# Kernel tuning notes

Measured on AMD Instinct MI355X. Metric: run time of the kernel, lower is better.

The kernel has to match this reference:

```python
import jax, jax.numpy as jnp
import numpy as np


def setup_inputs() -> dict:
    key = jax.random.key(0)
    kA, kB = jax.random.split(key)
    B, H, W, C = 1, 80, 80, 256  # NHWC backbone features; B must be 1 for the TF broadcast in the divide to be valid
    feature_A = jax.random.normal(kA, (B, H, W, C), dtype=jnp.float32)
    feature_B = jax.random.normal(kB, (B, H, W, C), dtype=jnp.float32)
    return {"feature_A": feature_A, "feature_B": feature_B}


def reference(feature_A, feature_B):
    # corr[b,i,j,k,l] = mean_c A[b,i,j,c] * B[b,k,l,c]
    # Expressed as a batched matmul instead of materializing the (H,W,H,W,C) intermediate.
    C = feature_A.shape[-1]
    corr = jnp.einsum('bijc,bklc->bijkl', feature_A, feature_B) / C  # [B,H,W,H,W]
    # penalty[b,i,j] = sqrt(sum_{k,l} corr^2)
    penalty = jnp.sqrt(jnp.sum(corr * corr, axis=(-1, -2)))  # [B,H,W]
    # Faithful to tf.math.divide: trailing-dim broadcasting of [B,H,W] against [B,H,W,H,W]
    # (valid because B == 1; penalty aligns to the (j,k,l) trailing axes exactly as in TF).
    return corr / penalty
```

## Files before the change

### kernel.cpp

```cpp
#include <hip/hip_runtime.h>

typedef __attribute__((ext_vector_type(8))) short bf16x8;
typedef __attribute__((ext_vector_type(4))) float f32x4;

#define M_TOT 6400
#define C_TOT 256
#define BM 128
#define BN 128
#define BK 32
#define GK_CHUNKS 20
#define GK_STEPS  10

#define VMCNT0 asm volatile("s_waitcnt vmcnt(0)" ::: "memory")
#define SBAR   __builtin_amdgcn_s_barrier()

__device__ __forceinline__ short f2bf(float f) {
    unsigned u = __float_as_uint(f);
    u = (u + 0x7fffu + ((u >> 16) & 1u)) >> 16;
    return (short)u;
}
__device__ __forceinline__ float bf2f(short s) {
    return __uint_as_float(((unsigned)(unsigned short)s) << 16);
}

__device__ __forceinline__ void gload16(const short* g, short* l) {
    __builtin_amdgcn_global_load_lds(
        (const __attribute__((address_space(1))) void*)g,
        (__attribute__((address_space(3))) void*)l, 16, 0, 0);
}


__global__ __launch_bounds__(256) void convert_bf16(const float* __restrict__ A,
                                                    const float* __restrict__ Bm,
                                                    short* __restrict__ Ab,
                                                    short* __restrict__ Bb)
{
    const int n8 = M_TOT * C_TOT / 8;
    for (int i = blockIdx.x * blockDim.x + threadIdx.x; i < 2 * n8;
         i += gridDim.x * blockDim.x) {
        const float* s = (i < n8) ? (A + (size_t)i * 8) : (Bm + (size_t)(i - n8) * 8);
        short* d       = (i < n8) ? (Ab + (size_t)i * 8) : (Bb + (size_t)(i - n8) * 8);
        const float4 v0 = reinterpret_cast<const float4*>(s)[0];
        const float4 v1 = reinterpret_cast<const float4*>(s)[1];
        bf16x8 w;
        w[0]=f2bf(v0.x); w[1]=f2bf(v0.y); w[2]=f2bf(v0.z); w[3]=f2bf(v0.w);
        w[4]=f2bf(v1.x); w[5]=f2bf(v1.y); w[6]=f2bf(v1.z); w[7]=f2bf(v1.w);
        *reinterpret_cast<bf16x8*>(d) = w;
    }
}

__global__ __launch_bounds__(256) void transpose_b(const float* __restrict__ Bm,
                                                   short* __restrict__ Bt)
{
    __shared__ __align__(16) short Lb[64][72];
    const int t  = threadIdx.x;
    const int n0 = blockIdx.x * 64;
    const int c0 = blockIdx.y * 64;
    const int r  = t >> 2;
    const int cb = (t & 3) * 16;

    const float4* src = reinterpret_cast<const float4*>(
        Bm + (size_t)(n0 + r) * C_TOT + c0 + cb);
    const float4 v0 = src[0], v1 = src[1], v2 = src[2], v3 = src[3];
    bf16x8 w0, w1;
    w0[0]=f2bf(v0.x); w0[1]=f2bf(v0.y); w0[2]=f2bf(v0.z); w0[3]=f2bf(v0.w);
    w0[4]=f2bf(v1.x); w0[5]=f2bf(v1.y); w0[6]=f2bf(v1.z); w0[7]=f2bf(v1.w);
    w1[0]=f2bf(v2.x); w1[1]=f2bf(v2.y); w1[2]=f2bf(v2.z); w1[3]=f2bf(v2.w);
    w1[4]=f2bf(v3.x); w1[5]=f2bf(v3.y); w1[6]=f2bf(v3.z); w1[7]=f2bf(v3.w);
    *reinterpret_cast<bf16x8*>(&Lb[r][cb])     = w0;
    *reinterpret_cast<bf16x8*>(&Lb[r][cb + 8]) = w1;
    __syncthreads();

    #pragma unroll
    for (int p = 0; p < 2; ++p) {
        const int q = t + p * 256;
        const int c = q >> 3;
        const int h = q & 7;
        bf16x8 w;
        #pragma unroll
        for (int j = 0; j < 8; ++j) w[j] = Lb[h * 8 + j][c];
        *reinterpret_cast<bf16x8*>(&Bt[(size_t)(c0 + c) * M_TOT + n0 + h * 8]) = w;
    }
}


__device__ __forceinline__ void stage_tiles_g(const short* __restrict__ A,
                                              const short* __restrict__ B,
                                              int m0, int n0, int k0,
                                              int lda, int ldb,
                                              short* As, short* Bs,
                                              int wave, int lane)
{
    #pragma unroll
    for (int t = 0; t < 2; ++t) {
        const int c  = (wave * 2 + t) * 64 + lane;
        const int r  = c >> 2;
        const int g  = c & 3;
        const int sg = g ^ ((r >> 1) & 3);
        gload16(A + (size_t)(m0 + r) * lda + k0 + sg * 8, As + (wave * 2 + t) * 512);
        gload16(B + (size_t)(n0 + r) * ldb + k0 + sg * 8, Bs + (wave * 2 + t) * 512);
    }
}

template<int KSTEPS>
__device__ __forceinline__ void gemm_tile_g(const short* __restrict__ A,
                                            const short* __restrict__ B,
                                            int m0, int n0, int kbase,
                                            int lda, int ldb, int tid,
                                            short (*Sm)[2][4096],
                                            f32x4 acc[4][4])
{
    const int lane = tid & 63;
    const int wave = tid >> 6;
    const int rl   = lane & 15;
    const int g_rd = lane >> 4;
    const int wr   = wave >> 1;
    const int wc   = wave & 1;

    stage_tiles_g(A, B, m0, n0, kbase, lda, ldb, &Sm[0][0][0], &Sm[0][1][0], wave, lane);
    VMCNT0; SBAR;

    #pragma unroll
    for (int kt = 0; kt < KSTEPS; ++kt) {
        const int cur = kt & 1;
        if (kt < KSTEPS - 1)
            stage_tiles_g(A, B, m0, n0, kbase + (kt + 1) * BK, lda, ldb,
                          &Sm[cur ^ 1][0][0], &Sm[cur ^ 1][1][0], wave, lane);

        bf16x8 af[4], bfr[4];
        #pragma unroll
        for (int mi = 0; mi < 4; ++mi) {
            const int r  = wr * 64 + mi * 16 + rl;
            const int sg = g_rd ^ ((r >> 1) & 3);
            af[mi] = *reinterpret_cast<const bf16x8*>(&Sm[cur][0][r * BK + sg * 8]);
        }
        #pragma unroll
        for (int ni = 0; ni < 4; ++ni) {
            const int r  = wc * 64 + ni * 16 + rl;
            const int sg = g_rd ^ ((r >> 1) & 3);
            bfr[ni] = *reinterpret_cast<const bf16x8*>(&Sm[cur][1][r * BK + sg * 8]);
        }
        #pragma unroll
        for (int mi = 0; mi < 4; ++mi)
            #pragma unroll
            for (int ni = 0; ni < 4; ++ni)
                acc[mi][ni] = __builtin_amdgcn_mfma_f32_16x16x32_bf16(
                    af[mi], bfr[ni], acc[mi][ni], 0, 0, 0);

        if (kt < KSTEPS - 1) { VMCNT0; SBAR; }
    }
}


__global__ __launch_bounds__(256) void gemm_G(const short* __restrict__ Bt,
                                              float* __restrict__ Gp)
{
    __shared__ __align__(16) short Sm[2][2][4096];
    const int tid = threadIdx.x;
    const int m0 = blockIdx.y * BM, n0 = blockIdx.x * BN;
    const int z  = blockIdx.z;
    f32x4 acc[4][4] = {};
    gemm_tile_g<GK_STEPS>(Bt, Bt, m0, n0, z * (M_TOT / GK_CHUNKS),
                          M_TOT, M_TOT, tid, Sm, acc);

    float* dst = Gp + (size_t)z * (C_TOT * C_TOT);
    const int lane = tid & 63, rl = lane & 15;
    const int wave = tid >> 6, wr = wave >> 1, wc = wave & 1;
    #pragma unroll
    for (int mi = 0; mi < 4; ++mi)
        #pragma unroll
        for (int i = 0; i < 4; ++i) {
            const int m = m0 + wr * 64 + mi * 16 + (lane >> 4) * 4 + i;
            #pragma unroll
            for (int ni = 0; ni < 4; ++ni)
                dst[m * C_TOT + n0 + wc * 64 + ni * 16 + rl] = acc[mi][ni][i];
        }
}

__global__ __launch_bounds__(256) void g_reduce(const float* __restrict__ Gp,
                                                short* __restrict__ Gb)
{
    const int i4 = blockIdx.x * 256 + threadIdx.x;
    float4 s = make_float4(0.f, 0.f, 0.f, 0.f);
    for (int z = 0; z < GK_CHUNKS; ++z) {
        const float4 v = reinterpret_cast<const float4*>(
            Gp + (size_t)z * (C_TOT * C_TOT))[i4];
        s.x += v.x; s.y += v.y; s.z += v.z; s.w += v.w;
    }
    short4 o;
    o.x = f2bf(s.x); o.y = f2bf(s.y); o.z = f2bf(s.z); o.w = f2bf(s.w);
    reinterpret_cast<short4*>(Gb)[i4] = o;
}

__global__ __launch_bounds__(256) void penalty_G(const short* __restrict__ Ab,
                                                 const short* __restrict__ Gb,
                                                 float* __restrict__ P)
{
    __shared__ __align__(16) short Sm[2][2][4096];
    __shared__ float q_lds[BM];
    const int tid = threadIdx.x;
    const int m0 = blockIdx.x * BM;
    const int lane = tid & 63, rl = lane & 15;
    const int wave = tid >> 6, wr = wave >> 1, wc = wave & 1;

    if (tid < BM) q_lds[tid] = 0.0f;
    __syncthreads();

    #pragma unroll
    for (int nt = 0; nt < 2; ++nt) {
        f32x4 acc[4][4] = {};
        gemm_tile_g<8>(Ab, Gb, m0, nt * BN, 0, C_TOT, C_TOT, tid, Sm, acc);
        const int n0 = nt * BN;
        #pragma unroll
        for (int mi = 0; mi < 4; ++mi)
            #pragma unroll
            for (int i = 0; i < 4; ++i) {
                const int m = m0 + wr * 64 + mi * 16 + (lane >> 4) * 4 + i;
                float s = 0.0f;
                #pragma unroll
                for (int ni = 0; ni < 4; ++ni) {
                    const int cp = n0 + wc * 64 + ni * 16 + rl;
                    s += acc[mi][ni][i] * bf2f(Ab[(size_t)m * C_TOT + cp]);
                }
                s += __shfl_xor(s, 1);
                s += __shfl_xor(s, 2);
                s += __shfl_xor(s, 4);
                s += __shfl_xor(s, 8);
                if (rl == 0) atomicAdd(&q_lds[m - m0], s);
            }
    }
    __syncthreads();
    if (tid < BM) P[m0 + tid] = q_lds[tid];
}


__global__ __launch_bounds__(256) void gemm_out(const short* __restrict__ Ab,
                                                const short* __restrict__ Bb,
                                                const float* __restrict__ P,
                                                float* __restrict__ out)
{
    __shared__ __align__(16) short Sm[2][2][4096];
    const int tid = threadIdx.x;
    const int lane = tid & 63, rl = lane & 15;
    const int wave = tid >> 6, wr = wave >> 1, wc = wave & 1;
    const int m0 = blockIdx.y * BM, n0 = blockIdx.x * BN;

    float rs[4];
    #pragma unroll
    for (int ni = 0; ni < 4; ++ni)
        rs[ni] = rsqrtf(P[n0 + wc * 64 + ni * 16 + rl]);

    f32x4 acc[4][4] = {};
    gemm_tile_g<8>(Ab, Bb, m0, n0, 0, C_TOT, C_TOT, tid, Sm, acc);

    SBAR;

    float* Es = reinterpret_cast<float*>(Sm) + wave * 1088;
    #pragma unroll
    for (int mi = 0; mi < 4; ++mi) {
        #pragma unroll
        for (int ni = 0; ni < 4; ++ni)
            #pragma unroll
            for (int i = 0; i < 4; ++i)
                Es[((lane >> 4) * 4 + i) * 68 + ni * 16 + rl] = acc[mi][ni][i] * rs[ni];
        #pragma unroll
        for (int it = 0; it < 4; ++it) {
            const int f   = it * 64 + lane;
            const int row = f >> 4;
            const int c4  = f & 15;
            const float4 v = *reinterpret_cast<const float4*>(&Es[row * 68 + c4 * 4]);
            const int m = m0 + wr * 64 + mi * 16 + row;
            *reinterpret_cast<float4*>(&out[(size_t)m * M_TOT + n0 + wc * 64 + c4 * 4]) = v;
        }
    }
}


__global__ __launch_bounds__(256) void gemm_penalty(const short* __restrict__ Ab,
                                                    const short* __restrict__ Bb,
                                                    float* __restrict__ P)
{
    __shared__ __align__(16) short Sm[2][2][4096];
    const int tid = threadIdx.x;
    const int m0 = blockIdx.y * BM, n0 = blockIdx.x * BN;
    f32x4 acc[4][4] = {};
    gemm_tile_g<8>(Ab, Bb, m0, n0, 0, C_TOT, C_TOT, tid, Sm, acc);

    const int lane = tid & 63, rl = lane & 15;
    const int wave = tid >> 6, wr = wave >> 1;
    #pragma unroll
    for (int mi = 0; mi < 4; ++mi) {
        #pragma unroll
        for (int i = 0; i < 4; ++i) {
            const int m = m0 + wr * 64 + mi * 16 + (lane >> 4) * 4 + i;
            float s = 0.0f;
            #pragma unroll
            for (int ni = 0; ni < 4; ++ni) {
                const float v = acc[mi][ni][i];
                s += v * v;
            }
            s += __shfl_xor(s, 1);
            s += __shfl_xor(s, 2);
            s += __shfl_xor(s, 4);
            s += __shfl_xor(s, 8);
            if (rl == 0) atomicAdd(&P[m], s);
        }
    }
}


__global__ __launch_bounds__(256) void corr_gemm(const float* __restrict__ A,
                                                 const float* __restrict__ Bm,
                                                 float* __restrict__ out,
                                                 float* __restrict__ penalty)
{
    __shared__ short As[BM * BK];
    __shared__ short Bs[BN * BK];

    const int tid  = threadIdx.x;
    const int lane = tid & 63;
    const int wave = tid >> 6;
    const int wr   = wave >> 1;
    const int wc   = wave & 1;
    const int m0   = blockIdx.y * BM;
    const int n0   = blockIdx.x * BN;
    const int g_rd = lane >> 4;
    const int rl   = lane & 15;

    f32x4 acc[4][4] = {};

    for (int k0 = 0; k0 < C_TOT; k0 += BK) {
        #pragma unroll
        for (int half = 0; half < 2; ++half) {
            const int cc = tid + half * 256;
            const int r  = cc >> 2;
            const int g  = cc & 3;
            const int sg = g ^ ((r >> 1) & 3);

            const float4* pa = reinterpret_cast<const float4*>(
                A + (size_t)(m0 + r) * C_TOT + k0 + g * 8);
            float4 a0 = pa[0], a1 = pa[1];
            bf16x8 wa;
            wa[0]=f2bf(a0.x); wa[1]=f2bf(a0.y); wa[2]=f2bf(a0.z); wa[3]=f2bf(a0.w);
            wa[4]=f2bf(a1.x); wa[5]=f2bf(a1.y); wa[6]=f2bf(a1.z); wa[7]=f2bf(a1.w);
            *reinterpret_cast<bf16x8*>(&As[r * BK + sg * 8]) = wa;

            const float4* pb = reinterpret_cast<const float4*>(
                Bm + (size_t)(n0 + r) * C_TOT + k0 + g * 8);
            float4 b0 = pb[0], b1 = pb[1];
            bf16x8 wb;
            wb[0]=f2bf(b0.x); wb[1]=f2bf(b0.y); wb[2]=f2bf(b0.z); wb[3]=f2bf(b0.w);
            wb[4]=f2bf(b1.x); wb[5]=f2bf(b1.y); wb[6]=f2bf(b1.z); wb[7]=f2bf(b1.w);
            *reinterpret_cast<bf16x8*>(&Bs[r * BK + sg * 8]) = wb;
        }
        __syncthreads();

        bf16x8 af[4], bfr[4];
        #pragma unroll
        for (int mi = 0; mi < 4; ++mi) {
            const int r  = wr * 64 + mi * 16 + rl;
            const int sg = g_rd ^ ((r >> 1) & 3);
            af[mi] = *reinterpret_cast<const bf16x8*>(&As[r * BK + sg * 8]);
        }
        #pragma unroll
        for (int ni = 0; ni < 4; ++ni) {
            const int r  = wc * 64 + ni * 16 + rl;
            const int sg = g_rd ^ ((r >> 1) & 3);
            bfr[ni] = *reinterpret_cast<const bf16x8*>(&Bs[r * BK + sg * 8]);
        }
        #pragma unroll
        for (int mi = 0; mi < 4; ++mi)
            #pragma unroll
            for (int ni = 0; ni < 4; ++ni)
                acc[mi][ni] = __builtin_amdgcn_mfma_f32_16x16x32_bf16(
                    af[mi], bfr[ni], acc[mi][ni], 0, 0, 0);
        __syncthreads();
    }

    const float inv_c = 1.0f / (float)C_TOT;
    #pragma unroll
    for (int mi = 0; mi < 4; ++mi) {
        #pragma unroll
        for (int i = 0; i < 4; ++i) {
            const int m = m0 + wr * 64 + mi * 16 + (lane >> 4) * 4 + i;
            float s = 0.0f;
            #pragma unroll
            for (int ni = 0; ni < 4; ++ni) {
                const float v = acc[mi][ni][i] * inv_c;
                out[(size_t)m * M_TOT + n0 + wc * 64 + ni * 16 + rl] = v;
                s += v * v;
            }
            s += __shfl_xor(s, 1);
            s += __shfl_xor(s, 2);
            s += __shfl_xor(s, 4);
            s += __shfl_xor(s, 8);
            if (rl == 0) atomicAdd(&penalty[m], s);
        }
    }
}

__global__ __launch_bounds__(256) void scale_k(float* __restrict__ out,
                                               const float* __restrict__ penalty)
{
    const unsigned cols4 = M_TOT / 4;
    const unsigned total = (unsigned)M_TOT * cols4;
    float4* o4 = reinterpret_cast<float4*>(out);
    const float4* p4 = reinterpret_cast<const float4*>(penalty);
    for (unsigned idx = blockIdx.x * blockDim.x + threadIdx.x; idx < total;
         idx += gridDim.x * blockDim.x) {
        const unsigned n4 = idx % cols4;
        const float4 p = p4[n4];
        float4 v = o4[idx];
        v.x *= rsqrtf(p.x);
        v.y *= rsqrtf(p.y);
        v.z *= rsqrtf(p.z);
        v.w *= rsqrtf(p.w);
        o4[idx] = v;
    }
}


extern "C" void kernel_launch(void* const* d_in, const int* in_sizes, int n_in,
                              void* d_out, int out_size, void* d_ws, size_t ws_size,
                              hipStream_t stream) {
    const float* A = (const float*)d_in[0];
    const float* B = (const float*)d_in[1];
    float* out     = (float*)d_out;

    const size_t mat_sh = (size_t)M_TOT * C_TOT;
    const size_t sz_ab  = mat_sh * sizeof(short);
    const size_t sz_gb  = (size_t)C_TOT * C_TOT * sizeof(short);
    const size_t sz_p   = (size_t)M_TOT * sizeof(float);
    const size_t sz_gp  = (size_t)GK_CHUNKS * C_TOT * C_TOT * sizeof(float);
    const size_t need_full = 3 * sz_ab + sz_gb + sz_p + sz_gp;
    const size_t need_mid  = 2 * sz_ab + sz_p;

    dim3 grid(M_TOT / BN, M_TOT / BM);

    if (ws_size >= need_full) {
        short* Ab = (short*)d_ws;
        short* Bb = Ab + mat_sh;
        short* Bt = Bb + mat_sh;
        short* Gb = Bt + mat_sh;
        float* P  = (float*)((char*)d_ws + 3 * sz_ab + sz_gb);
        float* Gp = (float*)((char*)d_ws + 3 * sz_ab + sz_gb + sz_p);

        convert_bf16<<<1600, 256, 0, stream>>>(A, B, Ab, Bb);
        transpose_b<<<dim3(M_TOT / 64, C_TOT / 64), 256, 0, stream>>>(B, Bt);
        gemm_G<<<dim3(2, 2, GK_CHUNKS), 256, 0, stream>>>(Bt, Gp);
        g_reduce<<<64, 256, 0, stream>>>(Gp, Gb);
        penalty_G<<<M_TOT / BM, 256, 0, stream>>>(Ab, Gb, P);
        gemm_out<<<grid, dim3(256), 0, stream>>>(Ab, Bb, P, out);
    } else if (ws_size >= need_mid) {
        short* Ab = (short*)d_ws;
        short* Bb = Ab + mat_sh;
        float* P  = (float*)(Bb + mat_sh);

        hipMemsetAsync(P, 0, sz_p, stream);
        convert_bf16<<<1600, 256, 0, stream>>>(A, B, Ab, Bb);
        gemm_penalty<<<grid, dim3(256), 0, stream>>>(Ab, Bb, P);
        gemm_out<<<grid, dim3(256), 0, stream>>>(Ab, Bb, P, out);
    } else {
        float* penalty = (float*)d_ws;
        hipMemsetAsync(penalty, 0, sz_p, stream);
        corr_gemm<<<grid, dim3(256), 0, stream>>>(A, B, out, penalty);
        scale_k<<<2048, 256, 0, stream>>>(out, penalty);
    }
}
```

Before: 89.86 us.

## Triple-buffer GEMM K-loop, remap gemm_out blocks across XCDs, fuse B conversion into transpose

```diff
diff --git a/kernel.cpp b/kernel.cpp
--- a/kernel.cpp
+++ b/kernel.cpp
@@ -8,10 +8,12 @@
 #define BM 128
 #define BN 128
 #define BK 32
+#define NTILE 50
 #define GK_CHUNKS 20
 #define GK_STEPS  10
 
 #define VMCNT0 asm volatile("s_waitcnt vmcnt(0)" ::: "memory")
+#define VMCNT4 asm volatile("s_waitcnt vmcnt(4)" ::: "memory")
 #define SBAR   __builtin_amdgcn_s_barrier()
 
 __device__ __forceinline__ short f2bf(float f) {
@@ -30,10 +32,25 @@
 }
 
 
-__global__ __launch_bounds__(256) void convert_bf16(const float* __restrict__ A,
-                                                    const float* __restrict__ Bm,
-                                                    short* __restrict__ Ab,
-                                                    short* __restrict__ Bb)
+__global__ __launch_bounds__(256) void convert_a(const float* __restrict__ A,
+                                                 short* __restrict__ Ab)
+{
+    const int n8 = M_TOT * C_TOT / 8;
+    for (int i = blockIdx.x * blockDim.x + threadIdx.x; i < n8;
+         i += gridDim.x * blockDim.x) {
+        const float4 v0 = reinterpret_cast<const float4*>(A + (size_t)i * 8)[0];
+        const float4 v1 = reinterpret_cast<const float4*>(A + (size_t)i * 8)[1];
+        bf16x8 w;
+        w[0]=f2bf(v0.x); w[1]=f2bf(v0.y); w[2]=f2bf(v0.z); w[3]=f2bf(v0.w);
+        w[4]=f2bf(v1.x); w[5]=f2bf(v1.y); w[6]=f2bf(v1.z); w[7]=f2bf(v1.w);
+        *reinterpret_cast<bf16x8*>(Ab + (size_t)i * 8) = w;
+    }
+}
+
+__global__ __launch_bounds__(256) void convert_ab(const float* __restrict__ A,
+                                                  const float* __restrict__ Bm,
+                                                  short* __restrict__ Ab,
+                                                  short* __restrict__ Bb)
 {
     const int n8 = M_TOT * C_TOT / 8;
     for (int i = blockIdx.x * blockDim.x + threadIdx.x; i < 2 * n8;
@@ -49,8 +66,9 @@
     }
 }
 
-__global__ __launch_bounds__(256) void transpose_b(const float* __restrict__ Bm,
-                                                   short* __restrict__ Bt)
+__global__ __launch_bounds__(256) void trans_b(const float* __restrict__ Bm,
+                                               short* __restrict__ Bb,
+                                               short* __restrict__ Bt)
 {
     __shared__ __align__(16) short Lb[64][72];
     const int t  = threadIdx.x;
@@ -69,6 +87,9 @@
     w1[4]=f2bf(v3.x); w1[5]=f2bf(v3.y); w1[6]=f2bf(v3.z); w1[7]=f2bf(v3.w);
     *reinterpret_cast<bf16x8*>(&Lb[r][cb])     = w0;
     *reinterpret_cast<bf16x8*>(&Lb[r][cb + 8]) = w1;
+    short* brow = Bb + (size_t)(n0 + r) * C_TOT + c0 + cb;
+    *reinterpret_cast<bf16x8*>(brow)     = w0;
+    *reinterpret_cast<bf16x8*>(brow + 8) = w1;
     __syncthreads();
 
     #pragma unroll
@@ -118,14 +139,18 @@
     const int wc   = wave & 1;
 
     stage_tiles_g(A, B, m0, n0, kbase, lda, ldb, &Sm[0][0][0], &Sm[0][1][0], wave, lane);
-    VMCNT0; SBAR;
+    if (KSTEPS > 1)
+        stage_tiles_g(A, B, m0, n0, kbase + BK, lda, ldb,
+                      &Sm[1][0][0], &Sm[1][1][0], wave, lane);
+    if (KSTEPS > 1) { VMCNT4; } else { VMCNT0; }
+    SBAR;
 
     #pragma unroll
     for (int kt = 0; kt < KSTEPS; ++kt) {
-        const int cur = kt & 1;
-        if (kt < KSTEPS - 1)
-            stage_tiles_g(A, B, m0, n0, kbase + (kt + 1) * BK, lda, ldb,
-                          &Sm[cur ^ 1][0][0], &Sm[cur ^ 1][1][0], wave, lane);
+        const int cur = kt % 3;
+        if (kt + 2 < KSTEPS)
+            stage_tiles_g(A, B, m0, n0, kbase + (kt + 2) * BK, lda, ldb,
+                          &Sm[(kt + 2) % 3][0][0], &Sm[(kt + 2) % 3][1][0], wave, lane);
 
         bf16x8 af[4], bfr[4];
         #pragma unroll
@@ -147,7 +172,10 @@
                 acc[mi][ni] = __builtin_amdgcn_mfma_f32_16x16x32_bf16(
                     af[mi], bfr[ni], acc[mi][ni], 0, 0, 0);
 
-        if (kt < KSTEPS - 1) { VMCNT0; SBAR; }
+        if (kt + 1 < KSTEPS) {
+            if (kt + 2 < KSTEPS) { VMCNT4; } else { VMCNT0; }
+            SBAR;
+        }
     }
 }
 
@@ -155,7 +183,7 @@
 __global__ __launch_bounds__(256) void gemm_G(const short* __restrict__ Bt,
                                               float* __restrict__ Gp)
 {
-    __shared__ __align__(16) short Sm[2][2][4096];
+    __shared__ __align__(16) short Sm[3][2][4096];
     const int tid = threadIdx.x;
     const int m0 = blockIdx.y * BM, n0 = blockIdx.x * BN;
     const int z  = blockIdx.z;
@@ -196,7 +224,7 @@
                                                  const short* __restrict__ Gb,
                                                  float* __restrict__ P)
 {
-    __shared__ __align__(16) short Sm[2][2][4096];
+    __shared__ __align__(16) short Sm[3][2][4096];
     __shared__ float q_lds[BM];
     const int tid = threadIdx.x;
     const int m0 = blockIdx.x * BM;
@@ -228,8 +256,8 @@
                 s += __shfl_xor(s, 8);
                 if (rl == 0) atomicAdd(&q_lds[m - m0], s);
             }
-    }
-    __syncthreads();
+        __syncthreads();
+    }
     if (tid < BM) P[m0 + tid] = q_lds[tid];
 }
 
@@ -239,11 +267,17 @@
                                                 const float* __restrict__ P,
                                                 float* __restrict__ out)
 {
-    __shared__ __align__(16) short Sm[2][2][4096];
+    __shared__ __align__(16) short Sm[3][2][4096];
     const int tid = threadIdx.x;
     const int lane = tid & 63, rl = lane & 15;
     const int wave = tid >> 6, wr = wave >> 1, wc = wave & 1;
-    const int m0 = blockIdx.y * BM, n0 = blockIdx.x * BN;
+
+    const int nwg = NTILE * NTILE, q = nwg >> 3, r = nwg & 7;
+    const int orig = blockIdx.x;
+    const int xcd = orig & 7, idx = orig >> 3;
+    const int wg = (xcd < r ? xcd * (q + 1) : r * (q + 1) + (xcd - r) * q) + idx;
+    const int m0 = (wg / NTILE) * BM;
+    const int n0 = (wg % NTILE) * BN;
 
     float rs[4];
     #pragma unroll
@@ -280,7 +314,7 @@
                                                     const short* __restrict__ Bb,
                                                     float* __restrict__ P)
 {
-    __shared__ __align__(16) short Sm[2][2][4096];
+    __shared__ __align__(16) short Sm[3][2][4096];
     const int tid = threadIdx.x;
     const int m0 = blockIdx.y * BM, n0 = blockIdx.x * BN;
     f32x4 acc[4][4] = {};
@@ -304,6 +338,47 @@
             s += __shfl_xor(s, 4);
             s += __shfl_xor(s, 8);
             if (rl == 0) atomicAdd(&P[m], s);
+        }
+    }
+}
+
+__global__ __launch_bounds__(256) void gemm_out_plain(const short* __restrict__ Ab,
+                                                      const short* __restrict__ Bb,
+                                                      const float* __restrict__ P,
+                                                      float* __restrict__ out)
+{
+    __shared__ __align__(16) short Sm[3][2][4096];
+    const int tid = threadIdx.x;
+    const int lane = tid & 63, rl = lane & 15;
+    const int wave = tid >> 6, wr = wave >> 1, wc = wave & 1;
+    const int m0 = blockIdx.y * BM, n0 = blockIdx.x * BN;
+
+    float rs[4];
+    #pragma unroll
+    for (int ni = 0; ni < 4; ++ni)
+        rs[ni] = rsqrtf(P[n0 + wc * 64 + ni * 16 + rl]);
+
+    f32x4 acc[4][4] = {};
+    gemm_tile_g<8>(Ab, Bb, m0, n0, 0, C_TOT, C_TOT, tid, Sm, acc);
+
+    SBAR;
+
+    float* Es = reinterpret_cast<float*>(Sm) + wave * 1088;
+    #pragma unroll
+    for (int mi = 0; mi < 4; ++mi) {
+        #pragma unroll
+        for (int ni = 0; ni < 4; ++ni)
+            #pragma unroll
+            for (int i = 0; i < 4; ++i)
+                Es[((lane >> 4) * 4 + i) * 68 + ni * 16 + rl] = acc[mi][ni][i] * rs[ni];
+        #pragma unroll
+        for (int it = 0; it < 4; ++it) {
+            const int f   = it * 64 + lane;
+            const int row = f >> 4;
+            const int c4  = f & 15;
+            const float4 v = *reinterpret_cast<const float4*>(&Es[row * 68 + c4 * 4]);
+            const int m = m0 + wr * 64 + mi * 16 + row;
+            *reinterpret_cast<float4*>(&out[(size_t)m * M_TOT + n0 + wc * 64 + c4 * 4]) = v;
         }
     }
 }
@@ -435,7 +510,7 @@
     const size_t need_full = 3 * sz_ab + sz_gb + sz_p + sz_gp;
     const size_t need_mid  = 2 * sz_ab + sz_p;
 
-    dim3 grid(M_TOT / BN, M_TOT / BM);
+    dim3 grid2(NTILE, NTILE);
 
     if (ws_size >= need_full) {
         short* Ab = (short*)d_ws;
@@ -445,25 +520,25 @@
         float* P  = (float*)((char*)d_ws + 3 * sz_ab + sz_gb);
         float* Gp = (float*)((char*)d_ws + 3 * sz_ab + sz_gb + sz_p);
 
-        convert_bf16<<<1600, 256, 0, stream>>>(A, B, Ab, Bb);
-        transpose_b<<<dim3(M_TOT / 64, C_TOT / 64), 256, 0, stream>>>(B, Bt);
+        convert_a<<<800, 256, 0, stream>>>(A, Ab);
+        trans_b<<<dim3(M_TOT / 64, C_TOT / 64), 256, 0, stream>>>(B, Bb, Bt);
         gemm_G<<<dim3(2, 2, GK_CHUNKS), 256, 0, stream>>>(Bt, Gp);
         g_reduce<<<64, 256, 0, stream>>>(Gp, Gb);
         penalty_G<<<M_TOT / BM, 256, 0, stream>>>(Ab, Gb, P);
-        gemm_out<<<grid, dim3(256), 0, stream>>>(Ab, Bb, P, out);
+        gemm_out<<<NTILE * NTILE, 256, 0, stream>>>(Ab, Bb, P, out);
     } else if (ws_size >= need_mid) {
         short* Ab = (short*)d_ws;
         short* Bb = Ab + mat_sh;
         float* P  = (float*)(Bb + mat_sh);
 
         hipMemsetAsync(P, 0, sz_p, stream);
-        convert_bf16<<<1600, 256, 0, stream>>>(A, B, Ab, Bb);
-        gemm_penalty<<<grid, dim3(256), 0, stream>>>(Ab, Bb, P);
-        gemm_out<<<grid, dim3(256), 0, stream>>>(Ab, Bb, P, out);
+        convert_ab<<<1600, 256, 0, stream>>>(A, B, Ab, Bb);
+        gemm_penalty<<<grid2, dim3(256), 0, stream>>>(Ab, Bb, P);
+        gemm_out_plain<<<grid2, dim3(256), 0, stream>>>(Ab, Bb, P, out);
     } else {
         float* penalty = (float*)d_ws;
         hipMemsetAsync(penalty, 0, sz_p, stream);
-        corr_gemm<<<grid, dim3(256), 0, stream>>>(A, B, out, penalty);
+        corr_gemm<<<grid2, dim3(256), 0, stream>>>(A, B, out, penalty);
         scale_k<<<2048, 256, 0, stream>>>(out, penalty);
     }
 }
```

Measured after the change: 85.52 us. -4.8%, faster.
